# Kernel tuning notes

Hardware: AMD Instinct MI355X
Metric: run time of the kernel (lower is better)

Reference implementation:

```python
import jax, jax.numpy as jnp
import numpy as np

B, N, C = 2, 4096, 1024   # batch, input_size (seq), channels
H, Dh = 16, 64            # nhead, head_dim = channels // nhead
K = 256                   # dim_k (Linformer projected length)
FF = 4096                 # dim_ff
DEPTH = 2
EPS = 1e-5


def setup_inputs() -> dict:
    key = jax.random.key(0)
    ks = jax.random.split(key, 16)
    s = 0.02
    return {
        "x": jax.random.normal(ks[0], (B, N, C), jnp.float32),
        # per-layer, per-head Q/K/V projections: Linear(channels -> head_dim, bias=False)
        "Wq": jax.random.normal(ks[1], (DEPTH, H, C, Dh), jnp.float32) * s,
        "Wk": jax.random.normal(ks[2], (DEPTH, H, C, Dh), jnp.float32) * s,
        "Wv": jax.random.normal(ks[3], (DEPTH, H, C, Dh), jnp.float32) * s,
        # output proj: Linear(nhead*head_dim -> channels) with bias
        "Wo": jax.random.normal(ks[4], (DEPTH, H * Dh, C), jnp.float32) * s,
        "bo": jax.random.normal(ks[5], (DEPTH, C), jnp.float32) * s,
        # layerwise-shared E_proj = Linear(input_size -> dim_k) applied along seq axis
        # (same object used for both K and V projections)
        "Ew": jax.random.normal(ks[6], (K, N), jnp.float32) * (1.0 / np.sqrt(N)),
        "Eb": jax.random.normal(ks[7], (K,), jnp.float32) * s,
        # FeedForward: Linear(C->FF), gelu, Linear(FF->C)
        "W1": jax.random.normal(ks[8], (DEPTH, C, FF), jnp.float32) * s,
        "b1": jax.random.normal(ks[9], (DEPTH, FF), jnp.float32) * s,
        "W2": jax.random.normal(ks[10], (DEPTH, FF, C), jnp.float32) * s,
        "b2": jax.random.normal(ks[11], (DEPTH, C), jnp.float32) * s,
        # post-residual LayerNorm params: [layer, {attn, ff}, channels]
        "ln_g": 1.0 + 0.02 * jax.random.normal(ks[12], (DEPTH, 2, C), jnp.float32),
        "ln_b": 0.02 * jax.random.normal(ks[13], (DEPTH, 2, C), jnp.float32),
    }


def _layernorm(x, g, b):
    mu = jnp.mean(x, axis=-1, keepdims=True)
    var = jnp.var(x, axis=-1, keepdims=True)
    return (x - mu) * jax.lax.rsqrt(var + EPS) * g + b


def reference(x, Wq, Wk, Wv, Wo, bo, Ew, Eb, W1, b1, W2, b2, ln_g, ln_b):
    scale = 1.0 / np.sqrt(Dh)
    for l in range(DEPTH):
        # ---- Linformer multi-head attention (dropout = identity at inference) ----
        q = jnp.einsum('bnc,hcd->bhnd', x, Wq[l])   # [B,H,N,Dh]
        k = jnp.einsum('bnc,hcd->bhnd', x, Wk[l])
        v = jnp.einsum('bnc,hcd->bhnd', x, Wv[l])
        # project seq axis n -> k with shared E_proj (K^T @ E, V^T @ E)
        kp = jnp.einsum('bhnd,kn->bhkd', k, Ew) + Eb[None, None, :, None]  # [B,H,K,Dh]
        vp = jnp.einsum('bhnd,kn->bhkd', v, Ew) + Eb[None, None, :, None]
        p = jax.nn.softmax(jnp.einsum('bhnd,bhkd->bhnk', q, kp) * scale, axis=-1)
        o = jnp.einsum('bhnk,bhkd->bhnd', p, vp)
        o = o.transpose(0, 2, 1, 3).reshape(B, N, H * Dh)  # concat heads
        attn_out = o @ Wo[l] + bo[l]
        x = _layernorm(x + attn_out, ln_g[l, 0], ln_b[l, 0])  # Residual post-norm
        # ---- FeedForward ----
        h = jax.nn.gelu(x @ W1[l] + b1[l], approximate=False)
        ff_out = h @ W2[l] + b2[l]
        x = _layernorm(x + ff_out, ln_g[l, 1], ln_b[l, 1])
    return x
```

## Files before the change

### kernel.cpp

```cpp
#include <hip/hip_runtime.h>
#include <hip/hip_bf16.h>
#include <math.h>

typedef __bf16 bf16x8 __attribute__((ext_vector_type(8)));
typedef float f32x4 __attribute__((ext_vector_type(4)));

__global__ void cvt_f32_bf16(const float* __restrict__ in, __bf16* __restrict__ out, long n) {
    long i = ((long)blockIdx.x * 256 + threadIdx.x) * 4;
    long stride = (long)gridDim.x * 1024;
    for (; i < n; i += stride) {
        float4 v = *(const float4*)(in + i);
        out[i + 0] = (__bf16)v.x;
        out[i + 1] = (__bf16)v.y;
        out[i + 2] = (__bf16)v.z;
        out[i + 3] = (__bf16)v.w;
    }
}

__global__ void transpose_cvt(const float* __restrict__ in, __bf16* __restrict__ out,
                              int ldin, int ldout, long inBS, long outBS) {
    __shared__ __bf16 tile[32][33];
    in  += (long)blockIdx.z * inBS;
    out += (long)blockIdx.z * outBS;
    int n0 = blockIdx.x * 32, m0 = blockIdx.y * 32;
    for (int i = threadIdx.y; i < 32; i += 8)
        tile[i][threadIdx.x] = (__bf16)in[(long)(m0 + i) * ldin + n0 + threadIdx.x];
    __syncthreads();
    for (int i = threadIdx.y; i < 32; i += 8)
        out[(long)(n0 + i) * ldout + m0 + threadIdx.x] = tile[threadIdx.x][i];
}

__global__ void transpose_bf16(const __bf16* __restrict__ in, __bf16* __restrict__ out,
                               int rows, int cols) {
    __shared__ __bf16 tile[32][33];
    in  += (long)blockIdx.z * rows * cols;
    out += (long)blockIdx.z * rows * cols;
    int c0 = blockIdx.x * 32, r0 = blockIdx.y * 32;
    for (int i = threadIdx.y; i < 32; i += 8)
        tile[i][threadIdx.x] = in[(long)(r0 + i) * cols + c0 + threadIdx.x];
    __syncthreads();
    for (int i = threadIdx.y; i < 32; i += 8)
        out[(long)(c0 + i) * rows + r0 + threadIdx.x] = tile[threadIdx.x][i];
}

__global__ void frag_cvt(const float* __restrict__ in, __bf16* __restrict__ out,
                         int K, int N, long inBS, long outBS) {
    __shared__ float tile[32][65];
    in  += (long)blockIdx.z * inBS;
    out += (long)blockIdx.z * outBS;
    const int n0 = blockIdx.x * 64, k0 = blockIdx.y * 32;
    for (int r = threadIdx.x >> 6; r < 32; r += 4)
        tile[r][threadIdx.x & 63] = in[(long)(k0 + r) * N + n0 + (threadIdx.x & 63)];
    __syncthreads();
    const int cl = threadIdx.x >> 6, lane = threadIdx.x & 63;
    const int nl = cl * 16 + (lane & 15);
    const int kl = (lane >> 4) * 8;
    const long chunk = (long)((n0 >> 4) + cl) * (K >> 5) + (k0 >> 5);
    bf16x8 v;
#pragma unroll
    for (int e = 0; e < 8; e++) v[e] = (__bf16)tile[kl + e][nl];
    *(bf16x8*)(out + chunk * 512 + lane * 8) = v;
}

template<int BN, bool ROWB, bool COLB, bool GELUF, bool RES, int OUT>
__global__ __launch_bounds__(512, 1) void gemm_bdir(
    const __bf16* __restrict__ A, int lda,
    const __bf16* __restrict__ Bf,
    void* __restrict__ outp, int ldc,
    const float* __restrict__ rowBias,
    const float* __restrict__ colBias,
    const float* __restrict__ res, int ldres,
    int K)
{
    constexpr int N_REP = BN >> 6;
    constexpr int M_REP = 8;
    __shared__ __bf16 Asm[3 * 256 * 64];

    const int tid = threadIdx.x, lane = tid & 63, wave = tid >> 6;
    const int l15 = lane & 15, l4 = lane >> 4;
    const int wm = wave >> 2, wn = wave & 3;

    int bx, by;
    {
        int id = blockIdx.y * gridDim.x + blockIdx.x;
        int xcd = id & 7, local = id >> 3;
        int nx = gridDim.y >> 3;
        by = xcd * nx + local / gridDim.x;
        bx = local % gridDim.x;
    }
    const long m0 = (long)bx * 256, n0 = (long)by * BN;

    const int srow = lane >> 3;
    const int gunit = ((lane & 7) ^ srow) << 3;
    const __bf16* Abp = A + (m0 + wave * 32 + srow) * (long)lda + gunit;

    auto stage = [&](int buf, int t) {
        __bf16* dst = Asm + buf * 16384 + wave * 2048;
        const __bf16* src = Abp + (long)t * 64;
#pragma unroll
        for (int j = 0; j < 4; j++)
            __builtin_amdgcn_global_load_lds(
                (const __attribute__((address_space(1))) unsigned int*)(src + (long)j * 8 * lda),
                (__attribute__((address_space(3))) unsigned int*)(dst + j * 512), 16, 0, 0);
    };

    const int kb5 = K >> 5;
    const int nblk0 = (int)(n0 >> 4) + wn * N_REP;

    f32x4 acc[M_REP][N_REP];
#pragma unroll
    for (int mi = 0; mi < M_REP; mi++)
#pragma unroll
        for (int ni = 0; ni < N_REP; ni++) acc[mi][ni] = (f32x4){0.f, 0.f, 0.f, 0.f};

    const int NT = K >> 6;
    stage(0, 0);
    stage(1, 1);
    int buf = 0, sbuf = 2;

    for (int t = 0; t < NT; t++) {
        if (t + 1 < NT) { asm volatile("s_waitcnt vmcnt(4)" ::: "memory"); }
        else            { asm volatile("s_waitcnt vmcnt(0)" ::: "memory"); }
        __builtin_amdgcn_s_barrier();

        bf16x8 bfv[2][N_REP];
#pragma unroll
        for (int ks = 0; ks < 2; ks++)
#pragma unroll
            for (int ni = 0; ni < N_REP; ni++)
                bfv[ks][ni] = *(const bf16x8*)(Bf + ((long)(nblk0 + ni) * kb5 + t * 2 + ks) * 512 + lane * 8);
        __builtin_amdgcn_sched_barrier(0);

        if (t + 2 < NT) stage(sbuf, t + 2);

        const __bf16* Abuf = Asm + buf * 16384;
#pragma unroll
        for (int ks = 0; ks < 2; ks++) {
            bf16x8 af[M_REP];
#pragma unroll
            for (int mi = 0; mi < M_REP; mi++)
                af[mi] = *(const bf16x8*)(Abuf + (wm * 128 + mi * 16 + l15) * 64 + (((ks * 4 + l4) ^ (l15 & 7)) << 3));
            __builtin_amdgcn_s_setprio(1);
#pragma unroll
            for (int mi = 0; mi < M_REP; mi++)
#pragma unroll
                for (int ni = 0; ni < N_REP; ni++)
                    acc[mi][ni] = __builtin_amdgcn_mfma_f32_16x16x32_bf16(af[mi], bfv[ks][ni], acc[mi][ni], 0, 0, 0);
            __builtin_amdgcn_s_setprio(0);
        }
        buf = (buf == 2) ? 0 : buf + 1;
        sbuf = (sbuf == 2) ? 0 : sbuf + 1;
    }

    float* outf = (float*)outp;
    __bf16* outb = (__bf16*)outp;
#pragma unroll
    for (int mi = 0; mi < M_REP; mi++)
#pragma unroll
        for (int ni = 0; ni < N_REP; ni++) {
            long gmb = m0 + wm * 128 + mi * 16 + l4 * 4;
            long gc  = n0 + wn * (BN / 4) + ni * 16 + l15;
#pragma unroll
            for (int i = 0; i < 4; i++) {
                long gm = gmb + i;
                float v = acc[mi][ni][i];
                if (ROWB)  v += rowBias[gm];
                if (COLB)  v += colBias[gc];
                if (GELUF) v = 0.5f * v * (1.f + erff(v * 0.70710678118f));
                if (RES)   v += res[gm * (long)ldres + gc];
                if (OUT == 0) outf[gm * (long)ldc + gc] = v;
                else          outb[gm * (long)ldc + gc] = (__bf16)v;
            }
        }
}

__global__ __launch_bounds__(256, 2) void gemm128_split(
    const __bf16* __restrict__ A, int lda, long aBS,
    const __bf16* __restrict__ Bt, int ldb, long bBS,
    float* __restrict__ P, long cBS, int ldc,
    int Ksplit, int S)
{
    __shared__ __bf16 Asm[128 * 64];
    __shared__ __bf16 Bsm[128 * 64];
    const int tid = threadIdx.x;
    const int lane = tid & 63, wave = tid >> 6;
    const int wm = wave >> 1, wn = wave & 1;
    const int l15 = lane & 15, l4 = lane >> 4;
    const long m0 = (long)blockIdx.x * 128, n0 = (long)blockIdx.y * 128;
    const long zb = blockIdx.z / S;
    const int  sp = blockIdx.z % S;
    A  += zb * aBS + (long)sp * Ksplit;
    Bt += zb * bBS + (long)sp * Ksplit;

    const int srow8 = lane >> 3;
    const int gunit = ((lane & 7) ^ srow8) << 3;
    const __bf16* Abase = A + (m0 + wave * 8 + srow8) * (long)lda + gunit;
    const __bf16* Bbase = Bt + (n0 + wave * 8 + srow8) * (long)ldb + gunit;
    __bf16* AsmW = Asm + wave * 8 * 64;
    __bf16* BsmW = Bsm + wave * 8 * 64;
    const int swz_r = l15 & 7;

    f32x4 acc[4][4];
#pragma unroll
    for (int mi = 0; mi < 4; mi++)
#pragma unroll
        for (int ni = 0; ni < 4; ni++) acc[mi][ni] = (f32x4){0.f, 0.f, 0.f, 0.f};

    for (int k0 = 0; k0 < Ksplit; k0 += 64) {
        __syncthreads();
#pragma unroll
        for (int p = 0; p < 4; p++) {
            __builtin_amdgcn_global_load_lds(
                (const __attribute__((address_space(1))) unsigned int*)(Abase + (long)p * 32 * lda + k0),
                (__attribute__((address_space(3))) unsigned int*)(AsmW + p * 32 * 64), 16, 0, 0);
            __builtin_amdgcn_global_load_lds(
                (const __attribute__((address_space(1))) unsigned int*)(Bbase + (long)p * 32 * ldb + k0),
                (__attribute__((address_space(3))) unsigned int*)(BsmW + p * 32 * 64), 16, 0, 0);
        }
        asm volatile("s_waitcnt vmcnt(0)" ::: "memory");
        __syncthreads();
#pragma unroll
        for (int ks = 0; ks < 2; ks++) {
            bf16x8 af[4], bfv[4];
#pragma unroll
            for (int mi = 0; mi < 4; mi++)
                af[mi] = *(const bf16x8*)(Asm + (wm * 64 + mi * 16 + l15) * 64 + (((ks * 4 + l4) ^ swz_r) << 3));
#pragma unroll
            for (int ni = 0; ni < 4; ni++)
                bfv[ni] = *(const bf16x8*)(Bsm + (wn * 64 + ni * 16 + l15) * 64 + (((ks * 4 + l4) ^ swz_r) << 3));
#pragma unroll
            for (int mi = 0; mi < 4; mi++)
#pragma unroll
                for (int ni = 0; ni < 4; ni++)
                    acc[mi][ni] = __builtin_amdgcn_mfma_f32_16x16x32_bf16(af[mi], bfv[ni], acc[mi][ni], 0, 0, 0);
        }
    }

    float* out = P + (long)blockIdx.z * cBS;
#pragma unroll
    for (int mi = 0; mi < 4; mi++)
#pragma unroll
        for (int ni = 0; ni < 4; ni++) {
            long gmb = m0 + wm * 64 + mi * 16 + l4 * 4;
            long gc  = n0 + wn * 64 + ni * 16 + l15;
#pragma unroll
            for (int i = 0; i < 4; i++)
                out[(gmb + i) * (long)ldc + gc] = acc[mi][ni][i];
        }
}

template<bool BIAS, bool TRANS>
__global__ __launch_bounds__(256) void reduce_partials(
    const float* __restrict__ P, __bf16* __restrict__ out,
    const float* __restrict__ bias, int S, int M, int N, long pBS)
{
    int b = blockIdx.z;
    long idx = ((long)blockIdx.x * 256 + threadIdx.x) * 4;
    if (idx >= (long)M * N) return;
    const float* Pb = P + (long)b * S * pBS + idx;
    float4 a = *(const float4*)Pb;
    for (int s = 1; s < S; s++) {
        float4 v = *(const float4*)(Pb + (long)s * pBS);
        a.x += v.x; a.y += v.y; a.z += v.z; a.w += v.w;
    }
    int m = (int)(idx / N), n = (int)(idx % N);
    if (BIAS) { float bv = bias[m]; a.x += bv; a.y += bv; a.z += bv; a.w += bv; }
    float av[4] = {a.x, a.y, a.z, a.w};
    if (!TRANS) {
        __bf16* o = out + (long)b * M * N + idx;
        o[0] = (__bf16)av[0]; o[1] = (__bf16)av[1]; o[2] = (__bf16)av[2]; o[3] = (__bf16)av[3];
    } else {
#pragma unroll
        for (int j = 0; j < 4; j++)
            out[(long)b * M * N + (long)(n + j) * M + m] = (__bf16)av[j];
    }
}

__global__ __launch_bounds__(256, 2) void attn_fused(
    const __bf16* __restrict__ Q, const __bf16* __restrict__ KP,
    const __bf16* __restrict__ VPt, __bf16* __restrict__ O)
{
    __shared__ __bf16 plds[4][4096];
    const int tid = threadIdx.x, lane = tid & 63, wave = tid >> 6;
    const int l15 = lane & 15, l4 = lane >> 4;
    const int h = blockIdx.y, b = blockIdx.z;
    const long row0 = (long)b * 4096 + (long)blockIdx.x * 64 + wave * 16;

    bf16x8 aq[2];
#pragma unroll
    for (int ks = 0; ks < 2; ks++)
        aq[ks] = *(const bf16x8*)(Q + (row0 + l15) * 1024 + h * 64 + ks * 32 + l4 * 8);

    f32x4 s[16];
#pragma unroll
    for (int f = 0; f < 16; f++) {
        f32x4 a = (f32x4){0.f, 0.f, 0.f, 0.f};
#pragma unroll
        for (int ks = 0; ks < 2; ks++) {
            bf16x8 bk = *(const bf16x8*)(KP + ((long)b * 256 + f * 16 + l15) * 1024 + h * 64 + ks * 32 + l4 * 8);
            a = __builtin_amdgcn_mfma_f32_16x16x32_bf16(aq[ks], bk, a, 0, 0, 0);
        }
        s[f] = a;
    }

    const float scale = 0.125f;
#pragma unroll
    for (int i = 0; i < 4; i++) {
        float m_ = -3.4e38f;
#pragma unroll
        for (int f = 0; f < 16; f++) { float v = s[f][i] * scale; s[f][i] = v; m_ = fmaxf(m_, v); }
#pragma unroll
        for (int msk = 1; msk < 16; msk <<= 1) m_ = fmaxf(m_, __shfl_xor(m_, msk));
        float su = 0.f;
#pragma unroll
        for (int f = 0; f < 16; f++) { float e = expf(s[f][i] - m_); s[f][i] = e; su += e; }
#pragma unroll
        for (int msk = 1; msk < 16; msk <<= 1) su += __shfl_xor(su, msk);
        float inv = 1.f / su;
#pragma unroll
        for (int f = 0; f < 16; f++) s[f][i] *= inv;
    }

    __bf16* pl = plds[wave];
#pragma unroll
    for (int f = 0; f < 16; f++)
#pragma unroll
        for (int i = 0; i < 4; i++) {
            int r = l4 * 4 + i, c = f * 16 + l15;
            int off = r * 256 + ((((c >> 3) ^ (r & 7)) << 3) | (c & 7));
            pl[off] = (__bf16)s[f][i];
        }

    f32x4 o[4];
#pragma unroll
    for (int f2 = 0; f2 < 4; f2++) o[f2] = (f32x4){0.f, 0.f, 0.f, 0.f};
#pragma unroll
    for (int ks = 0; ks < 8; ks++) {
        int kk = ks * 32 + l4 * 8;
        int off = l15 * 256 + (((kk >> 3) ^ (l15 & 7)) << 3);
        bf16x8 ap = *(const bf16x8*)(pl + off);
#pragma unroll
        for (int f2 = 0; f2 < 4; f2++) {
            bf16x8 bv = *(const bf16x8*)(VPt + ((long)b * 1024 + h * 64 + f2 * 16 + l15) * 256 + kk);
            o[f2] = __builtin_amdgcn_mfma_f32_16x16x32_bf16(ap, bv, o[f2], 0, 0, 0);
        }
    }
#pragma unroll
    for (int f2 = 0; f2 < 4; f2++)
#pragma unroll
        for (int i = 0; i < 4; i++)
            O[(row0 + l4 * 4 + i) * 1024 + h * 64 + f2 * 16 + l15] = (__bf16)o[f2][i];
}

__global__ __launch_bounds__(256) void ln_kernel(const float* __restrict__ y,
    const float* __restrict__ g, const float* __restrict__ b,
    float* __restrict__ xout, __bf16* __restrict__ xb)
{
    const int row = blockIdx.x;
    const int t = threadIdx.x;
    const float4 v = ((const float4*)(y + (long)row * 1024))[t];
    float s  = v.x + v.y + v.z + v.w;
    float ss = v.x * v.x + v.y * v.y + v.z * v.z + v.w * v.w;
#pragma unroll
    for (int m = 1; m < 64; m <<= 1) { s += __shfl_xor(s, m); ss += __shfl_xor(ss, m); }
    __shared__ float red[2][4];
    const int wave = t >> 6, lane = t & 63;
    if (lane == 0) { red[0][wave] = s; red[1][wave] = ss; }
    __syncthreads();
    s  = red[0][0] + red[0][1] + red[0][2] + red[0][3];
    ss = red[1][0] + red[1][1] + red[1][2] + red[1][3];
    const float mu = s * (1.f / 1024.f);
    const float var = ss * (1.f / 1024.f) - mu * mu;
    const float rs = rsqrtf(var + 1e-5f);
    const float4 gv = ((const float4*)g)[t];
    const float4 bv = ((const float4*)b)[t];
    float o0 = (v.x - mu) * rs * gv.x + bv.x;
    float o1 = (v.y - mu) * rs * gv.y + bv.y;
    float o2 = (v.z - mu) * rs * gv.z + bv.z;
    float o3 = (v.w - mu) * rs * gv.w + bv.w;
    float4 ov; ov.x = o0; ov.y = o1; ov.z = o2; ov.w = o3;
    ((float4*)(xout + (long)row * 1024))[t] = ov;
    __bf16* xr = xb + (long)row * 1024 + t * 4;
    xr[0] = (__bf16)o0; xr[1] = (__bf16)o1; xr[2] = (__bf16)o2; xr[3] = (__bf16)o3;
}

extern "C" void kernel_launch(void* const* d_in, const int* in_sizes, int n_in,
                              void* d_out, int out_size, void* d_ws, size_t ws_size,
                              hipStream_t stream) {
    const float* x   = (const float*)d_in[0];
    const float* Wq  = (const float*)d_in[1];
    const float* Wk  = (const float*)d_in[2];
    const float* Wv  = (const float*)d_in[3];
    const float* Wo  = (const float*)d_in[4];
    const float* bo  = (const float*)d_in[5];
    const float* Ew  = (const float*)d_in[6];
    const float* Eb  = (const float*)d_in[7];
    const float* W1  = (const float*)d_in[8];
    const float* b1  = (const float*)d_in[9];
    const float* W2  = (const float*)d_in[10];
    const float* b2  = (const float*)d_in[11];
    const float* lng = (const float*)d_in[12];
    const float* lnb = (const float*)d_in[13];
    float* xout = (float*)d_out;

    char* base = (char*)d_ws;
    size_t off = 0;
    auto alloc = [&](size_t bytes) { void* p = base + off; off += (bytes + 255) & ~(size_t)255; return p; };
    __bf16* Wkt = (__bf16*)alloc(2ll * 1024 * 1024 * 2);
    __bf16* Wvt = (__bf16*)alloc(2ll * 1024 * 1024 * 2);
    __bf16* Wqf = (__bf16*)alloc(2ll * 1024 * 1024 * 2);
    __bf16* Wof = (__bf16*)alloc(2ll * 1024 * 1024 * 2);
    __bf16* W1f = (__bf16*)alloc(2ll * 1024 * 4096 * 2);
    __bf16* W2f = (__bf16*)alloc(2ll * 1024 * 4096 * 2);
    __bf16* Ewb = (__bf16*)alloc(256ll * 4096 * 2);
    __bf16* xb  = (__bf16*)alloc(8192ll * 1024 * 2);
    __bf16* xbT = (__bf16*)alloc(2ll * 1024 * 4096 * 2);
    float*  y   = (float*) alloc(8192ll * 1024 * 4);
    __bf16* xp  = (__bf16*)alloc(2ll * 256 * 1024 * 2);
    __bf16* KPb = (__bf16*)alloc(2ll * 256 * 1024 * 2);
    __bf16* VPt = (__bf16*)alloc(2ll * 1024 * 256 * 2);
    __bf16* big = (__bf16*)alloc(8192ll * 4096 * 2);
    float*  xpP = (float*)big;
    float*  kpP = (float*)((char*)big + (16ll << 20));
    float*  vpP = (float*)((char*)big + (24ll << 20));
    __bf16* Qb  = big;
    __bf16* Ob  = big + (16ll << 20);
    __bf16* hbuf = big;

    cvt_f32_bf16<<<2048, 256, 0, stream>>>(x, xb, 8388608);
    cvt_f32_bf16<<<1024, 256, 0, stream>>>(Ew, Ewb, 1048576);
    transpose_cvt<<<dim3(2, 32, 32),  dim3(32, 8), 0, stream>>>(Wk, Wkt, 64, 1024, 65536, 65536);
    transpose_cvt<<<dim3(2, 32, 32),  dim3(32, 8), 0, stream>>>(Wv, Wvt, 64, 1024, 65536, 65536);
    frag_cvt<<<dim3(1, 32, 32),  256, 0, stream>>>(Wq, Wqf, 1024, 64, 65536, 65536);
    frag_cvt<<<dim3(16, 32, 2),  256, 0, stream>>>(Wo, Wof, 1024, 1024, 1048576, 1048576);
    frag_cvt<<<dim3(64, 32, 2),  256, 0, stream>>>(W1, W1f, 1024, 4096, 4194304, 4194304);
    frag_cvt<<<dim3(16, 128, 2), 256, 0, stream>>>(W2, W2f, 4096, 1024, 4194304, 4194304);

    for (int l = 0; l < 2; l++) {
        const __bf16* Wkt_l = Wkt + (long)l * 1048576;
        const __bf16* Wvt_l = Wvt + (long)l * 1048576;
        const __bf16* Wqf_l = Wqf + (long)l * 1048576;
        const __bf16* Wof_l = Wof + (long)l * 1048576;
        const __bf16* W1f_l = W1f + (long)l * 4194304;
        const __bf16* W2f_l = W2f + (long)l * 4194304;
        const float* res = (l == 0) ? x : xout;

        transpose_bf16<<<dim3(32, 128, 2), dim3(32, 8), 0, stream>>>(xb, xbT, 4096, 1024);
        gemm128_split<<<dim3(2, 8, 16), 256, 0, stream>>>(
            Ewb, 4096, 0, xbT, 4096, 4194304, xpP, 262144, 1024, 512, 8);
        reduce_partials<false, false><<<dim3(256, 1, 2), 256, 0, stream>>>(
            xpP, xp, nullptr, 8, 256, 1024, 262144);
        gemm128_split<<<dim3(2, 8, 8), 256, 0, stream>>>(
            xp, 1024, 262144, Wkt_l, 1024, 0, kpP, 262144, 1024, 256, 4);
        reduce_partials<true, false><<<dim3(256, 1, 2), 256, 0, stream>>>(
            kpP, KPb, Eb, 4, 256, 1024, 262144);
        gemm128_split<<<dim3(2, 8, 8), 256, 0, stream>>>(
            xp, 1024, 262144, Wvt_l, 1024, 0, vpP, 262144, 1024, 256, 4);
        reduce_partials<true, true><<<dim3(256, 1, 2), 256, 0, stream>>>(
            vpP, VPt, Eb, 4, 256, 1024, 262144);
        gemm_bdir<128, false, false, false, false, 1><<<dim3(32, 8), 512, 0, stream>>>(
            xb, 1024, Wqf_l, (void*)Qb, 1024, nullptr, nullptr, nullptr, 0, 1024);
        attn_fused<<<dim3(64, 16, 2), 256, 0, stream>>>(Qb, KPb, VPt, Ob);
        gemm_bdir<128, false, true, false, true, 0><<<dim3(32, 8), 512, 0, stream>>>(
            Ob, 1024, Wof_l, (void*)y, 1024, nullptr, bo + l * 1024, res, 1024, 1024);
        ln_kernel<<<8192, 256, 0, stream>>>(y, lng + (2 * l + 0) * 1024, lnb + (2 * l + 0) * 1024, xout, xb);
        gemm_bdir<256, false, true, true, false, 1><<<dim3(32, 16), 512, 0, stream>>>(
            xb, 1024, W1f_l, (void*)hbuf, 4096, nullptr, b1 + l * 4096, nullptr, 0, 1024);
        gemm_bdir<128, false, true, false, true, 0><<<dim3(32, 8), 512, 0, stream>>>(
            hbuf, 4096, W2f_l, (void*)y, 1024, nullptr, b2 + l * 1024, xout, 1024, 4096);
        ln_kernel<<<8192, 256, 0, stream>>>(y, lng + (2 * l + 1) * 1024, lnb + (2 * l + 1) * 1024, xout, xb);
    }
}
```

Before: 923.2 us.

## Shrink gemm_bdir K-step to 32 with smaller LDS and higher occupancy

Restructures the main GEMM so each iteration consumes a K-slice of 32 instead of 64. This cuts the triple-buffered A tile in LDS from 96KB to 48KB and fixes the per-wave N tile at 32 columns. Launch bounds go from 1 to 4 blocks per SM so several blocks can share a CU, and B fragments are now register double-buffered one iteration ahead. The FF1 GEMM moves from BN=256 to BN=128 with twice the grid. In exchange there are twice as many barriers per K, and the higher occupancy target may force register spills.

```diff
diff --git a/kernel.cpp b/kernel.cpp
--- a/kernel.cpp
+++ b/kernel.cpp
@@ -62,8 +62,8 @@
     *(bf16x8*)(out + chunk * 512 + lane * 8) = v;
 }
 
-template<int BN, bool ROWB, bool COLB, bool GELUF, bool RES, int OUT>
-__global__ __launch_bounds__(512, 1) void gemm_bdir(
+template<bool ROWB, bool COLB, bool GELUF, bool RES, int OUT>
+__global__ __launch_bounds__(512, 4) void gemm_bdir(
     const __bf16* __restrict__ A, int lda,
     const __bf16* __restrict__ Bf,
     void* __restrict__ outp, int ldc,
@@ -72,9 +72,7 @@
     const float* __restrict__ res, int ldres,
     int K)
 {
-    constexpr int N_REP = BN >> 6;
-    constexpr int M_REP = 8;
-    __shared__ __bf16 Asm[3 * 256 * 64];
+    __shared__ __bf16 Asm[3 * 8192];
 
     const int tid = threadIdx.x, lane = tid & 63, wave = tid >> 6;
     const int l15 = lane & 15, l4 = lane >> 4;
@@ -88,78 +86,84 @@
         by = xcd * nx + local / gridDim.x;
         bx = local % gridDim.x;
     }
-    const long m0 = (long)bx * 256, n0 = (long)by * BN;
-
-    const int srow = lane >> 3;
-    const int gunit = ((lane & 7) ^ srow) << 3;
-    const __bf16* Abp = A + (m0 + wave * 32 + srow) * (long)lda + gunit;
-
-    auto stage = [&](int buf, int t) {
-        __bf16* dst = Asm + buf * 16384 + wave * 2048;
-        const __bf16* src = Abp + (long)t * 64;
-#pragma unroll
-        for (int j = 0; j < 4; j++)
+    const long m0 = (long)bx * 256, n0 = (long)by * 128;
+
+    const __bf16* Abp = A + (m0 + wave * 32 + (lane >> 2)) * (long)lda
+                          + (((lane & 3) ^ ((lane >> 2) & 3)) << 3);
+    const int sdst = wave * 1024;
+
+    const int kb5 = K >> 5;
+    const int nblk0 = (int)(n0 >> 4) + wn * 2;
+    const int aoff = (wm * 128 + l15) * 32 + ((l4 ^ (l15 & 3)) << 3);
+
+    __bf16* pc = Asm;
+    __bf16* pn = Asm + 8192;
+    __bf16* ps = Asm + 16384;
+
+    f32x4 acc[8][2];
+#pragma unroll
+    for (int mi = 0; mi < 8; mi++) {
+        acc[mi][0] = (f32x4){0.f, 0.f, 0.f, 0.f};
+        acc[mi][1] = (f32x4){0.f, 0.f, 0.f, 0.f};
+    }
+
+    auto stage_to = [&](__bf16* dst, int t) {
+        const __bf16* src = Abp + (long)t * 32;
+#pragma unroll
+        for (int j = 0; j < 2; j++)
             __builtin_amdgcn_global_load_lds(
-                (const __attribute__((address_space(1))) unsigned int*)(src + (long)j * 8 * lda),
-                (__attribute__((address_space(3))) unsigned int*)(dst + j * 512), 16, 0, 0);
+                (const __attribute__((address_space(1))) unsigned int*)(src + (long)j * 16 * lda),
+                (__attribute__((address_space(3))) unsigned int*)(dst + sdst + j * 512), 16, 0, 0);
     };
-
-    const int kb5 = K >> 5;
-    const int nblk0 = (int)(n0 >> 4) + wn * N_REP;
-
-    f32x4 acc[M_REP][N_REP];
-#pragma unroll
-    for (int mi = 0; mi < M_REP; mi++)
-#pragma unroll
-        for (int ni = 0; ni < N_REP; ni++) acc[mi][ni] = (f32x4){0.f, 0.f, 0.f, 0.f};
-
-    const int NT = K >> 6;
-    stage(0, 0);
-    stage(1, 1);
-    int buf = 0, sbuf = 2;
-
-    for (int t = 0; t < NT; t++) {
-        if (t + 1 < NT) { asm volatile("s_waitcnt vmcnt(4)" ::: "memory"); }
-        else            { asm volatile("s_waitcnt vmcnt(0)" ::: "memory"); }
+    auto bload = [&](int t, bf16x8 (&B)[2]) {
+#pragma unroll
+        for (int ni = 0; ni < 2; ni++)
+            B[ni] = *(const bf16x8*)(Bf + ((long)(nblk0 + ni) * kb5 + t) * 512 + lane * 8);
+    };
+    auto iter = [&](int t, bf16x8 (&Bc)[2], bf16x8 (&Bn)[2],
+                    bool do_stage, bool do_bload, bool w4) {
+        if (w4) { asm volatile("s_waitcnt vmcnt(4)" ::: "memory"); }
+        else    { asm volatile("s_waitcnt vmcnt(2)" ::: "memory"); }
         __builtin_amdgcn_s_barrier();
-
-        bf16x8 bfv[2][N_REP];
-#pragma unroll
-        for (int ks = 0; ks < 2; ks++)
-#pragma unroll
-            for (int ni = 0; ni < N_REP; ni++)
-                bfv[ks][ni] = *(const bf16x8*)(Bf + ((long)(nblk0 + ni) * kb5 + t * 2 + ks) * 512 + lane * 8);
         __builtin_amdgcn_sched_barrier(0);
-
-        if (t + 2 < NT) stage(sbuf, t + 2);
-
-        const __bf16* Abuf = Asm + buf * 16384;
-#pragma unroll
-        for (int ks = 0; ks < 2; ks++) {
-            bf16x8 af[M_REP];
-#pragma unroll
-            for (int mi = 0; mi < M_REP; mi++)
-                af[mi] = *(const bf16x8*)(Abuf + (wm * 128 + mi * 16 + l15) * 64 + (((ks * 4 + l4) ^ (l15 & 7)) << 3));
-            __builtin_amdgcn_s_setprio(1);
-#pragma unroll
-            for (int mi = 0; mi < M_REP; mi++)
-#pragma unroll
-                for (int ni = 0; ni < N_REP; ni++)
-                    acc[mi][ni] = __builtin_amdgcn_mfma_f32_16x16x32_bf16(af[mi], bfv[ks][ni], acc[mi][ni], 0, 0, 0);
-            __builtin_amdgcn_s_setprio(0);
-        }
-        buf = (buf == 2) ? 0 : buf + 1;
-        sbuf = (sbuf == 2) ? 0 : sbuf + 1;
-    }
+        if (do_stage) stage_to(ps, t + 2);
+        if (do_bload) bload(t + 1, Bn);
+        bf16x8 af[8];
+#pragma unroll
+        for (int mi = 0; mi < 8; mi++)
+            af[mi] = *(const bf16x8*)(pc + aoff + mi * 512);
+        __builtin_amdgcn_s_setprio(1);
+#pragma unroll
+        for (int mi = 0; mi < 8; mi++) {
+            acc[mi][0] = __builtin_amdgcn_mfma_f32_16x16x32_bf16(af[mi], Bc[0], acc[mi][0], 0, 0, 0);
+            acc[mi][1] = __builtin_amdgcn_mfma_f32_16x16x32_bf16(af[mi], Bc[1], acc[mi][1], 0, 0, 0);
+        }
+        __builtin_amdgcn_s_setprio(0);
+        __bf16* tmp = pc; pc = pn; pn = ps; ps = tmp;
+    };
+
+    const int NT = K >> 5;
+    bf16x8 Ba[2], Bb[2];
+    stage_to(pc, 0);
+    stage_to(pn, 1);
+    bload(0, Ba);
+
+    int t = 0;
+    for (; t + 2 < NT; t += 2) {
+        iter(t,     Ba, Bb, true, true, true);
+        iter(t + 1, Bb, Ba, true, true, true);
+    }
+    iter(NT - 2, Ba, Bb, false, true,  true);
+    iter(NT - 1, Bb, Ba, false, false, false);
 
     float* outf = (float*)outp;
     __bf16* outb = (__bf16*)outp;
 #pragma unroll
-    for (int mi = 0; mi < M_REP; mi++)
-#pragma unroll
-        for (int ni = 0; ni < N_REP; ni++) {
+    for (int mi = 0; mi < 8; mi++)
+#pragma unroll
+        for (int ni = 0; ni < 2; ni++) {
             long gmb = m0 + wm * 128 + mi * 16 + l4 * 4;
-            long gc  = n0 + wn * (BN / 4) + ni * 16 + l15;
+            long gc  = n0 + wn * 32 + ni * 16 + l15;
 #pragma unroll
             for (int i = 0; i < 4; i++) {
                 long gm = gmb + i;
@@ -458,15 +462,15 @@
             xp, 1024, 262144, Wvt_l, 1024, 0, vpP, 262144, 1024, 256, 4);
         reduce_partials<true, true><<<dim3(256, 1, 2), 256, 0, stream>>>(
             vpP, VPt, Eb, 4, 256, 1024, 262144);
-        gemm_bdir<128, false, false, false, false, 1><<<dim3(32, 8), 512, 0, stream>>>(
+        gemm_bdir<false, false, false, false, 1><<<dim3(32, 8), 512, 0, stream>>>(
             xb, 1024, Wqf_l, (void*)Qb, 1024, nullptr, nullptr, nullptr, 0, 1024);
         attn_fused<<<dim3(64, 16, 2), 256, 0, stream>>>(Qb, KPb, VPt, Ob);
-        gemm_bdir<128, false, true, false, true, 0><<<dim3(32, 8), 512, 0, stream>>>(
+        gemm_bdir<false, true, false, true, 0><<<dim3(32, 8), 512, 0, stream>>>(
             Ob, 1024, Wof_l, (void*)y, 1024, nullptr, bo + l * 1024, res, 1024, 1024);
         ln_kernel<<<8192, 256, 0, stream>>>(y, lng + (2 * l + 0) * 1024, lnb + (2 * l + 0) * 1024, xout, xb);
-        gemm_bdir<256, false, true, true, false, 1><<<dim3(32, 16), 512, 0, stream>>>(
+        gemm_bdir<false, true, true, false, 1><<<dim3(32, 32), 512, 0, stream>>>(
             xb, 1024, W1f_l, (void*)hbuf, 4096, nullptr, b1 + l * 4096, nullptr, 0, 1024);
-        gemm_bdir<128, false, true, false, true, 0><<<dim3(32, 8), 512, 0, stream>>>(
+        gemm_bdir<false, true, false, true, 0><<<dim3(32, 8), 512, 0, stream>>>(
             hbuf, 4096, W2f_l, (void*)y, 1024, nullptr, b2 + l * 1024, xout, 1024, 4096);
         ln_kernel<<<8192, 256, 0, stream>>>(y, lng + (2 * l + 1) * 1024, lnb + (2 * l + 1) * 1024, xout, xb);
     }
```

Measured after the change: 1.452 ms. 1.57x slower.
